# Performance work log

Measured on AMD Instinct MI355X. Metric: run time of the kernel, lower is better.

## Reference

```python
import jax, jax.numpy as jnp
import numpy as np

NUM_EXPERTS = 16
HIDDEN = 1024
INTERMEDIATE = 768
T = 64
TOPK = 2


def setup_inputs() -> dict:
    key = jax.random.key(0)
    k1, k2, k3, k4, k5 = jax.random.split(key, 5)
    x = jax.random.normal(k1, (T, HIDDEN), dtype=jnp.float32)
    topk_ids = jax.random.randint(k2, (T, TOPK), 0, NUM_EXPERTS)
    topk_weight = jax.random.uniform(k3, (T, TOPK), dtype=jnp.float32)
    # w13 = cat([gate_proj.weight, up_proj.weight], dim=0) per expert -> [E, 2*d_ff, d]
    w13_weight = jax.random.normal(k4, (NUM_EXPERTS, 2 * INTERMEDIATE, HIDDEN), dtype=jnp.float32) * 0.02
    # down_proj.weight per expert -> [E, d, d_ff]
    w2_weight = jax.random.normal(k5, (NUM_EXPERTS, HIDDEN, INTERMEDIATE), dtype=jnp.float32) * 0.02
    return {"x": x, "topk_ids": topk_ids, "topk_weight": topk_weight,
            "w13_weight": w13_weight, "w2_weight": w2_weight}


def reference(x, topk_ids, topk_weight, w13_weight, w2_weight):
    # Gather full expert weights per (token, expert-slot) -- faithful to the
    # naive torch indexing self.w13_weight[topk_ids].
    w13 = w13_weight[topk_ids]                 # [t, a, 2*d_ff, d]
    w1, w3 = jnp.split(w13, 2, axis=2)          # each [t, a, d_ff, d]
    w2 = w2_weight[topk_ids]                   # [t, a, d, d_ff]
    x1 = jnp.einsum('ti,taoi->tao', x, w1)      # gate
    x1 = jax.nn.silu(x1)
    x3 = jnp.einsum('ti,taoi->tao', x, w3)      # up
    expert_outs = jnp.einsum('tao,taio->tai', x1 * x3, w2)  # down
    return jnp.einsum('tai,ta->ti', expert_outs, topk_weight.astype(expert_outs.dtype))
```

## Files before the change

### kernel.cpp

```cpp
#include <hip/hip_runtime.h>
#include <math.h>

#define NUM_EXPERTS 16
#define HIDDEN 1024
#define INTER 768
#define TOKENS 64
#define TOPK 2
#define NPAIRS (TOKENS*TOPK)
#define GRP 8
#define NZ 2

__device__ inline void build_plist(const int* __restrict__ topk_ids, int e,
                                   int tid, int* s_plist, int* s_np) {
    if (tid < 64) {
        const int lane = tid;
        int m0 = (topk_ids[lane]      == e);
        int m1 = (topk_ids[lane + 64] == e);
        unsigned long long b0 = __ballot(m0);
        unsigned long long b1 = __ballot(m1);
        int n0 = __popcll(b0);
        unsigned long long below = (lane == 0) ? 0ull : ((1ull << lane) - 1ull);
        if (m0) s_plist[__popcll(b0 & below)]      = lane;
        if (m1) s_plist[n0 + __popcll(b1 & below)] = lane + 64;
        if (lane == 0) *s_np = n0 + __popcll(b1);
    }
    __syncthreads();
}

__global__ __launch_bounds__(256) void moe_pass1(
    const float* __restrict__ x,
    const int*   __restrict__ topk_ids,
    const float* __restrict__ w13,
    float*       __restrict__ h)
{
    const int e    = blockIdx.y;
    const int z    = blockIdx.z;
    const int wave = threadIdx.x >> 6;
    const int o0   = blockIdx.x * 16 + wave * 4;
    const int tid  = threadIdx.x;
    const int lane = tid & 63;

    __shared__ int   s_plist[NPAIRS];
    __shared__ int   s_np;
    __shared__ float s_x[GRP][HIDDEN];

    build_plist(topk_ids, e, tid, s_plist, &s_np);
    const int np = s_np;

    for (int g = z; g * GRP < np; g += NZ) {
        const int gnp = min(GRP, np - g * GRP);
        for (int idx = tid; idx < gnp * (HIDDEN/4); idx += 256) {
            int tau = idx / (HIDDEN/4);
            int c   = idx % (HIDDEN/4);
            int t   = s_plist[g*GRP + tau] >> 1;
            *(float4*)(&s_x[tau][c*4]) = *(const float4*)(x + (size_t)t*HIDDEN + c*4);
        }
        __syncthreads();

        #pragma unroll
        for (int rr = 0; rr < 4; rr += 2) {
            const int oA = o0 + rr;
            const int oB = o0 + rr + 1;
            const float* w1A = w13 + ((size_t)e * (2*INTER) + oA) * HIDDEN;
            const float* w3A = w13 + ((size_t)e * (2*INTER) + INTER + oA) * HIDDEN;
            const float* w1B = w13 + ((size_t)e * (2*INTER) + oB) * HIDDEN;
            const float* w3B = w13 + ((size_t)e * (2*INTER) + INTER + oB) * HIDDEN;
            float4 a1A[4], a3A[4], a1B[4], a3B[4];
            #pragma unroll
            for (int j = 0; j < 4; ++j) {
                a1A[j] = *(const float4*)(w1A + lane*4 + 256*j);
                a3A[j] = *(const float4*)(w3A + lane*4 + 256*j);
                a1B[j] = *(const float4*)(w1B + lane*4 + 256*j);
                a3B[j] = *(const float4*)(w3B + lane*4 + 256*j);
            }
            for (int tau = 0; tau < gnp; ++tau) {
                float acc1A = 0.f, acc3A = 0.f, acc1B = 0.f, acc3B = 0.f;
                #pragma unroll
                for (int j = 0; j < 4; ++j) {
                    const float4 xv = *(const float4*)(&s_x[tau][lane*4 + 256*j]);
                    acc1A += a1A[j].x*xv.x + a1A[j].y*xv.y + a1A[j].z*xv.z + a1A[j].w*xv.w;
                    acc3A += a3A[j].x*xv.x + a3A[j].y*xv.y + a3A[j].z*xv.z + a3A[j].w*xv.w;
                    acc1B += a1B[j].x*xv.x + a1B[j].y*xv.y + a1B[j].z*xv.z + a1B[j].w*xv.w;
                    acc3B += a3B[j].x*xv.x + a3B[j].y*xv.y + a3B[j].z*xv.z + a3B[j].w*xv.w;
                }
                #pragma unroll
                for (int m = 32; m > 0; m >>= 1) {
                    acc1A += __shfl_xor(acc1A, m, 64);
                    acc3A += __shfl_xor(acc3A, m, 64);
                    acc1B += __shfl_xor(acc1B, m, 64);
                    acc3B += __shfl_xor(acc3B, m, 64);
                }
                if (lane == 0) {
                    int p = s_plist[g*GRP + tau];
                    float gA = acc1A / (1.f + expf(-acc1A));
                    float gB = acc1B / (1.f + expf(-acc1B));
                    h[(size_t)p * INTER + oA] = gA * acc3A;
                    h[(size_t)p * INTER + oB] = gB * acc3B;
                }
            }
        }
        __syncthreads();
    }
}

__global__ __launch_bounds__(256) void moe_pass2(
    const int*   __restrict__ topk_ids,
    const float* __restrict__ w2,
    const float* __restrict__ h,
    float*       __restrict__ y)
{
    const int e    = blockIdx.y;
    const int z    = blockIdx.z;
    const int wave = threadIdx.x >> 6;
    const int i0   = blockIdx.x * 16 + wave * 4;
    const int tid  = threadIdx.x;
    const int lane = tid & 63;

    __shared__ int   s_plist[NPAIRS];
    __shared__ int   s_np;
    __shared__ float s_h[GRP][INTER];

    build_plist(topk_ids, e, tid, s_plist, &s_np);
    const int np = s_np;

    for (int g = z; g * GRP < np; g += NZ) {
        const int gnp = min(GRP, np - g * GRP);
        for (int idx = tid; idx < gnp * (INTER/4); idx += 256) {
            int tau = idx / (INTER/4);
            int c   = idx % (INTER/4);
            int p   = s_plist[g*GRP + tau];
            *(float4*)(&s_h[tau][c*4]) = *(const float4*)(h + (size_t)p*INTER + c*4);
        }
        __syncthreads();

        #pragma unroll
        for (int rr = 0; rr < 4; rr += 2) {
            const int iA = i0 + rr;
            const int iB = i0 + rr + 1;
            const float* wA = w2 + ((size_t)e * HIDDEN + iA) * INTER;
            const float* wB = w2 + ((size_t)e * HIDDEN + iB) * INTER;
            float4 aA[3], aB[3];
            #pragma unroll
            for (int j = 0; j < 3; ++j) {
                aA[j] = *(const float4*)(wA + lane*4 + 256*j);
                aB[j] = *(const float4*)(wB + lane*4 + 256*j);
            }
            for (int tau = 0; tau < gnp; ++tau) {
                float accA = 0.f, accB = 0.f;
                #pragma unroll
                for (int j = 0; j < 3; ++j) {
                    const float4 hv = *(const float4*)(&s_h[tau][lane*4 + 256*j]);
                    accA += aA[j].x*hv.x + aA[j].y*hv.y + aA[j].z*hv.z + aA[j].w*hv.w;
                    accB += aB[j].x*hv.x + aB[j].y*hv.y + aB[j].z*hv.z + aB[j].w*hv.w;
                }
                #pragma unroll
                for (int m = 32; m > 0; m >>= 1) {
                    accA += __shfl_xor(accA, m, 64);
                    accB += __shfl_xor(accB, m, 64);
                }
                if (lane == 0) {
                    int p = s_plist[g*GRP + tau];
                    y[(size_t)p * HIDDEN + iA] = accA;
                    y[(size_t)p * HIDDEN + iB] = accB;
                }
            }
        }
        __syncthreads();
    }
}

__global__ __launch_bounds__(256) void moe_combine(
    const float* __restrict__ tw,
    const float* __restrict__ y,
    float*       __restrict__ out)
{
    int idx = blockIdx.x * 256 + threadIdx.x;
    int t = idx / (HIDDEN/4);
    int c = idx % (HIDDEN/4);
    float w0 = tw[t*2+0], w1 = tw[t*2+1];
    float4 a = *(const float4*)(y + (size_t)(2*t  )*HIDDEN + c*4);
    float4 b = *(const float4*)(y + (size_t)(2*t+1)*HIDDEN + c*4);
    float4 o;
    o.x = w0*a.x + w1*b.x;
    o.y = w0*a.y + w1*b.y;
    o.z = w0*a.z + w1*b.z;
    o.w = w0*a.w + w1*b.w;
    *(float4*)(out + (size_t)t*HIDDEN + c*4) = o;
}

extern "C" void kernel_launch(void* const* d_in, const int* in_sizes, int n_in,
                              void* d_out, int out_size, void* d_ws, size_t ws_size,
                              hipStream_t stream) {
    const float* x   = (const float*)d_in[0];
    const int*   ids = (const int*)  d_in[1];
    const float* tw  = (const float*)d_in[2];
    const float* w13 = (const float*)d_in[3];
    const float* w2  = (const float*)d_in[4];
    float* out = (float*)d_out;

    float* h = (float*)d_ws;
    float* y = h + (size_t)NPAIRS * INTER;

    dim3 g1(INTER/16, NUM_EXPERTS, NZ);
    moe_pass1<<<g1, 256, 0, stream>>>(x, ids, w13, h);

    dim3 g2(HIDDEN/16, NUM_EXPERTS, NZ);
    moe_pass2<<<g2, 256, 0, stream>>>(ids, w2, h, y);

    moe_combine<<<(TOKENS*HIDDEN/4)/256, 256, 0, stream>>>(tw, y, out);
}
```

Before: 54.97 us.

## Split each weight row across 16 lanes and read activations directly from global

Both expert GEMV kernels now give each 16-lane group one weight row. Each lane holds 16 (or 12) float4 in registers, which shortens the shuffle reduction to 4 steps. The shared-memory activation staging, the z-split of token groups and the block barriers are removed, and x/h rows are read straight from global (through the cache) for each token. Pass1 pairs gate and up rows in adjacent 16-lane groups and combines them with one extra shuffle. The grids double in x for pass1 and lose the z dimension, so more blocks each keep fewer rows, and expert blocks with no tokens exit early.

```diff
diff --git a/kernel.cpp b/kernel.cpp
--- a/kernel.cpp
+++ b/kernel.cpp
@@ -7,8 +7,10 @@
 #define TOKENS 64
 #define TOPK 2
 #define NPAIRS (TOKENS*TOPK)
-#define GRP 8
-#define NZ 2
+
+__device__ __forceinline__ float dot4(float4 a, float4 b) {
+    return a.x*b.x + a.y*b.y + a.z*b.z + a.w*b.w;
+}
 
 __device__ inline void build_plist(const int* __restrict__ topk_ids, int e,
                                    int tid, int* s_plist, int* s_np) {
@@ -34,72 +36,48 @@
     float*       __restrict__ h)
 {
     const int e    = blockIdx.y;
-    const int z    = blockIdx.z;
-    const int wave = threadIdx.x >> 6;
-    const int o0   = blockIdx.x * 16 + wave * 4;
     const int tid  = threadIdx.x;
+    const int wave = tid >> 6;
     const int lane = tid & 63;
+    const int g    = lane >> 4;
+    const int l16  = lane & 15;
 
-    __shared__ int   s_plist[NPAIRS];
-    __shared__ int   s_np;
-    __shared__ float s_x[GRP][HIDDEN];
+    const int row  = blockIdx.x * 8 + wave * 2 + (g >> 1);
+    const int mat  = g & 1;
 
+    __shared__ int s_plist[NPAIRS];
+    __shared__ int s_np;
     build_plist(topk_ids, e, tid, s_plist, &s_np);
     const int np = s_np;
+    if (np == 0) return;
 
-    for (int g = z; g * GRP < np; g += NZ) {
-        const int gnp = min(GRP, np - g * GRP);
-        for (int idx = tid; idx < gnp * (HIDDEN/4); idx += 256) {
-            int tau = idx / (HIDDEN/4);
-            int c   = idx % (HIDDEN/4);
-            int t   = s_plist[g*GRP + tau] >> 1;
-            *(float4*)(&s_x[tau][c*4]) = *(const float4*)(x + (size_t)t*HIDDEN + c*4);
+    const float* wrow = w13 + ((size_t)e * (2*INTER) + (size_t)mat * INTER + row) * HIDDEN + l16 * 4;
+    float4 w[16];
+    #pragma unroll
+    for (int j = 0; j < 16; ++j)
+        w[j] = *(const float4*)(wrow + j * 64);
+
+    for (int s = 0; s < np; ++s) {
+        const int p = s_plist[s];
+        const float* xrow = x + (size_t)(p >> 1) * HIDDEN + l16 * 4;
+        float a0 = 0.f, a1 = 0.f, a2 = 0.f, a3 = 0.f;
+        #pragma unroll
+        for (int j = 0; j < 16; j += 4) {
+            a0 += dot4(w[j+0], *(const float4*)(xrow + (j+0) * 64));
+            a1 += dot4(w[j+1], *(const float4*)(xrow + (j+1) * 64));
+            a2 += dot4(w[j+2], *(const float4*)(xrow + (j+2) * 64));
+            a3 += dot4(w[j+3], *(const float4*)(xrow + (j+3) * 64));
         }
-        __syncthreads();
-
-        #pragma unroll
-        for (int rr = 0; rr < 4; rr += 2) {
-            const int oA = o0 + rr;
-            const int oB = o0 + rr + 1;
-            const float* w1A = w13 + ((size_t)e * (2*INTER) + oA) * HIDDEN;
-            const float* w3A = w13 + ((size_t)e * (2*INTER) + INTER + oA) * HIDDEN;
-            const float* w1B = w13 + ((size_t)e * (2*INTER) + oB) * HIDDEN;
-            const float* w3B = w13 + ((size_t)e * (2*INTER) + INTER + oB) * HIDDEN;
-            float4 a1A[4], a3A[4], a1B[4], a3B[4];
-            #pragma unroll
-            for (int j = 0; j < 4; ++j) {
-                a1A[j] = *(const float4*)(w1A + lane*4 + 256*j);
-                a3A[j] = *(const float4*)(w3A + lane*4 + 256*j);
-                a1B[j] = *(const float4*)(w1B + lane*4 + 256*j);
-                a3B[j] = *(const float4*)(w3B + lane*4 + 256*j);
-            }
-            for (int tau = 0; tau < gnp; ++tau) {
-                float acc1A = 0.f, acc3A = 0.f, acc1B = 0.f, acc3B = 0.f;
-                #pragma unroll
-                for (int j = 0; j < 4; ++j) {
-                    const float4 xv = *(const float4*)(&s_x[tau][lane*4 + 256*j]);
-                    acc1A += a1A[j].x*xv.x + a1A[j].y*xv.y + a1A[j].z*xv.z + a1A[j].w*xv.w;
-                    acc3A += a3A[j].x*xv.x + a3A[j].y*xv.y + a3A[j].z*xv.z + a3A[j].w*xv.w;
-                    acc1B += a1B[j].x*xv.x + a1B[j].y*xv.y + a1B[j].z*xv.z + a1B[j].w*xv.w;
-                    acc3B += a3B[j].x*xv.x + a3B[j].y*xv.y + a3B[j].z*xv.z + a3B[j].w*xv.w;
-                }
-                #pragma unroll
-                for (int m = 32; m > 0; m >>= 1) {
-                    acc1A += __shfl_xor(acc1A, m, 64);
-                    acc3A += __shfl_xor(acc3A, m, 64);
-                    acc1B += __shfl_xor(acc1B, m, 64);
-                    acc3B += __shfl_xor(acc3B, m, 64);
-                }
-                if (lane == 0) {
-                    int p = s_plist[g*GRP + tau];
-                    float gA = acc1A / (1.f + expf(-acc1A));
-                    float gB = acc1B / (1.f + expf(-acc1B));
-                    h[(size_t)p * INTER + oA] = gA * acc3A;
-                    h[(size_t)p * INTER + oB] = gB * acc3B;
-                }
-            }
+        float acc = (a0 + a1) + (a2 + a3);
+        acc += __shfl_xor(acc, 1, 64);
+        acc += __shfl_xor(acc, 2, 64);
+        acc += __shfl_xor(acc, 4, 64);
+        acc += __shfl_xor(acc, 8, 64);
+        float other = __shfl_xor(acc, 16, 64);
+        if (mat == 0 && l16 == 0) {
+            float gate = acc / (1.f + expf(-acc));
+            h[(size_t)p * INTER + row] = gate * other;
         }
-        __syncthreads();
     }
 }
 
@@ -110,62 +88,45 @@
     float*       __restrict__ y)
 {
     const int e    = blockIdx.y;
-    const int z    = blockIdx.z;
-    const int wave = threadIdx.x >> 6;
-    const int i0   = blockIdx.x * 16 + wave * 4;
     const int tid  = threadIdx.x;
+    const int wave = tid >> 6;
     const int lane = tid & 63;
+    const int g    = lane >> 4;
+    const int l16  = lane & 15;
 
-    __shared__ int   s_plist[NPAIRS];
-    __shared__ int   s_np;
-    __shared__ float s_h[GRP][INTER];
+    const int row  = blockIdx.x * 16 + wave * 4 + g;
 
+    __shared__ int s_plist[NPAIRS];
+    __shared__ int s_np;
     build_plist(topk_ids, e, tid, s_plist, &s_np);
     const int np = s_np;
+    if (np == 0) return;
 
-    for (int g = z; g * GRP < np; g += NZ) {
-        const int gnp = min(GRP, np - g * GRP);
-        for (int idx = tid; idx < gnp * (INTER/4); idx += 256) {
-            int tau = idx / (INTER/4);
-            int c   = idx % (INTER/4);
-            int p   = s_plist[g*GRP + tau];
-            *(float4*)(&s_h[tau][c*4]) = *(const float4*)(h + (size_t)p*INTER + c*4);
+    const float* wrow = w2 + ((size_t)e * HIDDEN + row) * INTER + l16 * 4;
+    float4 w[12];
+    #pragma unroll
+    for (int j = 0; j < 12; ++j)
+        w[j] = *(const float4*)(wrow + j * 64);
+
+    for (int s = 0; s < np; ++s) {
+        const int p = s_plist[s];
+        const float* hrow = h + (size_t)p * INTER + l16 * 4;
+        float a0 = 0.f, a1 = 0.f, a2 = 0.f, a3 = 0.f;
+        #pragma unroll
+        for (int j = 0; j < 12; j += 4) {
+            a0 += dot4(w[j+0], *(const float4*)(hrow + (j+0) * 64));
+            a1 += dot4(w[j+1], *(const float4*)(hrow + (j+1) * 64));
+            a2 += dot4(w[j+2], *(const float4*)(hrow + (j+2) * 64));
+            a3 += dot4(w[j+3], *(const float4*)(hrow + (j+3) * 64));
         }
-        __syncthreads();
-
-        #pragma unroll
-        for (int rr = 0; rr < 4; rr += 2) {
-            const int iA = i0 + rr;
-            const int iB = i0 + rr + 1;
-            const float* wA = w2 + ((size_t)e * HIDDEN + iA) * INTER;
-            const float* wB = w2 + ((size_t)e * HIDDEN + iB) * INTER;
-            float4 aA[3], aB[3];
-            #pragma unroll
-            for (int j = 0; j < 3; ++j) {
-                aA[j] = *(const float4*)(wA + lane*4 + 256*j);
-                aB[j] = *(const float4*)(wB + lane*4 + 256*j);
-            }
-            for (int tau = 0; tau < gnp; ++tau) {
-                float accA = 0.f, accB = 0.f;
-                #pragma unroll
-                for (int j = 0; j < 3; ++j) {
-                    const float4 hv = *(const float4*)(&s_h[tau][lane*4 + 256*j]);
-                    accA += aA[j].x*hv.x + aA[j].y*hv.y + aA[j].z*hv.z + aA[j].w*hv.w;
-                    accB += aB[j].x*hv.x + aB[j].y*hv.y + aB[j].z*hv.z + aB[j].w*hv.w;
-                }
-                #pragma unroll
-                for (int m = 32; m > 0; m >>= 1) {
-                    accA += __shfl_xor(accA, m, 64);
-                    accB += __shfl_xor(accB, m, 64);
-                }
-                if (lane == 0) {
-                    int p = s_plist[g*GRP + tau];
-                    y[(size_t)p * HIDDEN + iA] = accA;
-                    y[(size_t)p * HIDDEN + iB] = accB;
-                }
-            }
+        float acc = (a0 + a1) + (a2 + a3);
+        acc += __shfl_xor(acc, 1, 64);
+        acc += __shfl_xor(acc, 2, 64);
+        acc += __shfl_xor(acc, 4, 64);
+        acc += __shfl_xor(acc, 8, 64);
+        if (l16 == 0) {
+            y[(size_t)p * HIDDEN + row] = acc;
         }
-        __syncthreads();
     }
 }
 
@@ -201,10 +162,10 @@
     float* h = (float*)d_ws;
     float* y = h + (size_t)NPAIRS * INTER;
 
-    dim3 g1(INTER/16, NUM_EXPERTS, NZ);
+    dim3 g1(INTER/8, NUM_EXPERTS);
     moe_pass1<<<g1, 256, 0, stream>>>(x, ids, w13, h);
 
-    dim3 g2(HIDDEN/16, NUM_EXPERTS, NZ);
+    dim3 g2(HIDDEN/16, NUM_EXPERTS);
     moe_pass2<<<g2, 256, 0, stream>>>(ids, w2, h, y);
 
     moe_combine<<<(TOKENS*HIDDEN/4)/256, 256, 0, stream>>>(tw, y, out);
```

New measurement: 78.90 us. 1.44x slower.
